# Optimization experiments

Hardware: AMD Instinct MI355X
Metric: run time of the kernel (lower is better)

The kernel has to match this reference:

```python
import jax, jax.numpy as jnp
import numpy as np

B, P, ENC, DEC, EMB, ATT, V, L = 32, 196, 2048, 512, 512, 512, 32000, 21
T = L - 1  # decode steps


def setup_inputs() -> dict:
    key = jax.random.key(0)
    ks = jax.random.split(key, 20)
    u = lambda k, s, a=0.1: jax.random.uniform(k, s, jnp.float32, -a, a)
    lens = jax.random.randint(ks[1], (B, 1), 5, L + 1)
    lens = lens.at[0, 0].set(L)  # force max_decode_len == T (static)
    return {
        'encoder_out': jax.random.normal(ks[0], (B, P, ENC), jnp.float32),
        'encoded_captions': jax.random.randint(ks[2], (B, L), 0, V),
        'caption_lengths': lens,
        'emb_W': u(ks[3], (V, EMB)),
        'W_ea': u(ks[4], (ATT, ENC), 0.02), 'b_ea': jnp.zeros((ATT,)),
        'W_da': u(ks[5], (ATT, DEC), 0.02), 'b_da': jnp.zeros((ATT,)),
        'w_fa': u(ks[6], (1, ATT), 0.02), 'b_fa': jnp.zeros((1,)),
        'W_ih': u(ks[7], (4 * DEC, EMB + ENC), 0.02), 'b_ih': jnp.zeros((4 * DEC,)),
        'W_hh': u(ks[8], (4 * DEC, DEC), 0.02), 'b_hh': jnp.zeros((4 * DEC,)),
        'W_h0': u(ks[9], (DEC, ENC), 0.02), 'b_h0': jnp.zeros((DEC,)),
        'W_c0': u(ks[10], (DEC, ENC), 0.02), 'b_c0': jnp.zeros((DEC,)),
        'W_fb': u(ks[11], (ENC, DEC), 0.02), 'b_fb': jnp.zeros((ENC,)),
        'W_fc': u(ks[12], (V, DEC)), 'b_fc': jnp.zeros((V,)),
    }


def reference(encoder_out, encoded_captions, caption_lengths, emb_W,
              W_ea, b_ea, W_da, b_da, w_fa, b_fa,
              W_ih, b_ih, W_hh, b_hh, W_h0, b_h0, W_c0, b_c0,
              W_fb, b_fb, W_fc, b_fc):
    # sort by caption length descending (as in torch forward)
    lens = caption_lengths[:, 0]
    sort_ind = jnp.argsort(-lens)
    lens_s = lens[sort_ind]
    enc = encoder_out[sort_ind]          # [B,P,ENC]
    caps = encoded_captions[sort_ind]    # [B,L]
    dec_lens = lens_s - 1

    mean_enc = enc.mean(axis=1)
    h0 = mean_enc @ W_h0.T + b_h0
    c0 = mean_enc @ W_c0.T + b_c0

    att1 = jnp.einsum('bpe,ae->bpa', enc, W_ea) + b_ea  # precompute encoder attn proj
    embs = emb_W[caps]                                   # [B,L,EMB]
    emb_seq = jnp.transpose(embs[:, :T], (1, 0, 2))      # [T,B,EMB] (teacher forcing)
    mask_seq = jnp.arange(T)[:, None] < dec_lens[None, :]  # [T,B]

    def step(carry, xs):
        h, c = carry
        emb_t, m = xs  # [B,EMB], [B] bool; m emulates shrinking batch_size_t
        att2 = h @ W_da.T + b_da
        e = jnp.maximum(att1 + att2[:, None, :], 0.0) @ w_fa[0] + b_fa[0]  # [B,P]
        alpha = jax.nn.softmax(e, axis=1)
        awe = jnp.einsum('bp,bpe->be', alpha, enc)
        gate = jax.nn.sigmoid(h @ W_fb.T + b_fb)
        x = jnp.concatenate([emb_t, gate * awe], axis=1)
        g = x @ W_ih.T + b_ih + h @ W_hh.T + b_hh
        i, f, gg, o = jnp.split(g, 4, axis=1)
        c_new = jax.nn.sigmoid(f) * c + jax.nn.sigmoid(i) * jnp.tanh(gg)
        h_new = jax.nn.sigmoid(o) * jnp.tanh(c_new)
        preds = h_new @ W_fc.T + b_fc  # dropout in eval mode (identity)
        mf = m[:, None]
        h = jnp.where(mf, h_new, h)
        c = jnp.where(mf, c_new, c)
        preds = preds * mf.astype(preds.dtype)
        alpha = alpha * mf.astype(alpha.dtype)
        return (h, c), (preds, alpha)

    _, (preds, alphas) = jax.lax.scan(step, (h0, c0), (emb_seq, mask_seq))
    predictions = jnp.transpose(preds, (1, 0, 2))  # [B,T,V]
    alphas = jnp.transpose(alphas, (1, 0, 2))      # [B,T,P]
    return predictions, alphas
```

## Files before the change

### kernel.cpp

```cpp
#include <hip/hip_runtime.h>
#include <hip/hip_bf16.h>
#include <cstddef>

#define NB 32
#define NP 196
#define NE 2048
#define ND 512
#define NV 32000
#define NL 21
#define NT 20

typedef __attribute__((ext_vector_type(8))) short short8;
typedef __attribute__((ext_vector_type(4))) float f32x4;

__device__ __forceinline__ unsigned short f2b(float f) {
    __hip_bfloat16 h = __float2bfloat16(f);
    return *reinterpret_cast<unsigned short*>(&h);
}
__device__ __forceinline__ float b2f_lo(unsigned int u) {
    union { unsigned int i; float f; } v; v.i = u << 16; return v.f;
}
__device__ __forceinline__ float b2f_hi(unsigned int u) {
    union { unsigned int i; float f; } v; v.i = u & 0xffff0000u; return v.f;
}


__global__ void k_sort(const int* __restrict__ lens, int* __restrict__ sind, int* __restrict__ dlens,
                       int* __restrict__ rowmap, int* __restrict__ mpad)
{
    int i = threadIdx.x;
    if (i < NB) {
        int li = lens[i];
        int r = 0;
        for (int j = 0; j < NB; ++j) {
            int lj = lens[j];
            if (lj > li || (lj == li && j < i)) ++r;
        }
        sind[r] = i;
        dlens[r] = li - 1;
    }
    __syncthreads();
    if (i == 0) {
        int c = 0;
        for (int t = 0; t < NT; ++t)
            for (int b = 0; b < NB; ++b)
                if (t < dlens[b]) rowmap[c++] = t * NB + b;
        int pad = (c + 63) & ~63;
        for (int r = c; r < pad; ++r) rowmap[r] = -1;
        mpad[0] = pad;
    }
}

__global__ __launch_bounds__(256) void k_mean(const float* __restrict__ enc, const int* __restrict__ sind,
                                              float* __restrict__ mean_enc)
{
    int b = blockIdx.y;
    int k = blockIdx.x * 256 + threadIdx.x;
    const float* e = enc + (size_t)sind[b] * NP * NE + k;
    float s0 = 0.f, s1 = 0.f, s2 = 0.f, s3 = 0.f;
    for (int p = 0; p < NP; p += 4) {
        s0 += e[(size_t)(p + 0) * NE];
        s1 += e[(size_t)(p + 1) * NE];
        s2 += e[(size_t)(p + 2) * NE];
        s3 += e[(size_t)(p + 3) * NE];
    }
    mean_enc[(size_t)b * NE + k] = (s0 + s1 + s2 + s3) * (1.0f / NP);
}

__global__ __launch_bounds__(256) void k_zero(const int* __restrict__ dlens, float* __restrict__ out)
{
    int b = blockIdx.x / NT, t = blockIdx.x % NT;
    if (t < dlens[b]) return;
    float4 z = {0.f, 0.f, 0.f, 0.f};
    float4* row = (float4*)(out + ((size_t)b * NT + t) * NV);
    for (int i = threadIdx.x; i < NV / 4; i += 256) row[i] = z;
}

__global__ __launch_bounds__(256) void gemm_skinny_split(
    const float* __restrict__ A0, const float* __restrict__ W0a, const float* __restrict__ W0b,
    float* __restrict__ spart)
{
    __shared__ float As[32][32];
    __shared__ float Ws[64][33];
    int n0 = blockIdx.x * 64;
    int ks = blockIdx.y;
    int tid = threadIdx.x;
    int lb = tid / 8, lkq = tid % 8;
    int b4 = (tid / 32) * 4, nl = (tid % 32) * 2;
    float acc[4][2] = {};
    for (int kt = ks * 256; kt < ks * 256 + 256; kt += 32) {
        float4 a4 = *reinterpret_cast<const float4*>(A0 + (size_t)lb * NE + kt + lkq * 4);
        As[lkq * 4 + 0][lb] = a4.x; As[lkq * 4 + 1][lb] = a4.y;
        As[lkq * 4 + 2][lb] = a4.z; As[lkq * 4 + 3][lb] = a4.w;
        #pragma unroll
        for (int r = 0; r < 2; ++r) {
            int s = tid + r * 256;
            int n_l = s / 8, kq = s % 8;
            int ng = n0 + n_l;
            const float* wrow = (ng < 512) ? (W0a + (size_t)ng * NE)
                                           : (W0b + (size_t)(ng - 512) * NE);
            float4 w4 = *reinterpret_cast<const float4*>(wrow + kt + kq * 4);
            Ws[n_l][kq * 4 + 0] = w4.x; Ws[n_l][kq * 4 + 1] = w4.y;
            Ws[n_l][kq * 4 + 2] = w4.z; Ws[n_l][kq * 4 + 3] = w4.w;
        }
        __syncthreads();
        #pragma unroll
        for (int k = 0; k < 32; ++k) {
            float4 av = *reinterpret_cast<const float4*>(&As[k][b4]);
            float w0 = Ws[nl][k], w1 = Ws[nl + 1][k];
            acc[0][0] += av.x * w0; acc[0][1] += av.x * w1;
            acc[1][0] += av.y * w0; acc[1][1] += av.y * w1;
            acc[2][0] += av.z * w0; acc[2][1] += av.z * w1;
            acc[3][0] += av.w * w0; acc[3][1] += av.w * w1;
        }
        __syncthreads();
    }
    float* Cp = spart + (size_t)ks * NB * 1024;
    #pragma unroll
    for (int j = 0; j < 2; ++j)
        #pragma unroll
        for (int i = 0; i < 4; ++i)
            Cp[(size_t)(b4 + i) * 1024 + n0 + nl + j] = acc[i][j];
}

__global__ __launch_bounds__(256) void k_hc0(
    const float* __restrict__ spart, const float* __restrict__ ba, const float* __restrict__ bb,
    float* __restrict__ hc, float* __restrict__ xh)
{
    int b = blockIdx.x;
    for (int ng = threadIdx.x; ng < 1024; ng += 256) {
        float s = (ng < 512) ? ba[ng] : bb[ng - 512];
        #pragma unroll
        for (int ks = 0; ks < 8; ++ks)
            s += spart[(size_t)ks * NB * 1024 + (size_t)b * 1024 + ng];
        hc[(size_t)b * 1024 + ng] = s;
        if (ng < 512) xh[(size_t)b * 3072 + 2560 + ng] = s;
    }
}

__global__ __launch_bounds__(256) void gemm_att1_mfma(
    const float* __restrict__ enc, const float* __restrict__ W_ea,
    const float* __restrict__ bias, unsigned short* __restrict__ att1B,
    const int* __restrict__ sind)
{
    int fid = blockIdx.x;
    int c = fid & 7, x = (fid >> 3) & 7, pg = fid >> 6;
    int p = pg * 8 + c;
    if (p >= 98) return;
    int bm0 = p * 64, bn0 = x * 64;
    __shared__ unsigned short As[64][40];
    __shared__ unsigned short Bs[64][40];
    int tid = threadIdx.x;
    int w = tid >> 6, lane = tid & 63;
    int srow = tid >> 2, schunk = (tid & 3) * 8;
    int mg = bm0 + srow;
    int bidx = mg / NP, pp = mg - bidx * NP;
    const float* arow = enc + ((size_t)sind[bidx] * NP + pp) * NE + schunk;
    const float* brow = W_ea + (size_t)(bn0 + srow) * NE + schunk;
// ... 24 lines not shown
        }
        __syncthreads();
    }
    int crow = bm0 + w * 16 + (lane >> 4) * 4;
    int ccol0 = lane & 15;
    #pragma unroll
    for (int n = 0; n < 4; ++n) {
        int col = bn0 + n * 16 + ccol0;
        float bb2 = bias[col];
        #pragma unroll
        for (int i = 0; i < 4; ++i)
            att1B[(size_t)(crow + i) * ND + col] = f2b(acc[n][i] + bb2);
    }
}

__global__ __launch_bounds__(256) void gemm_preds_mfma(
    const unsigned short* __restrict__ hseqB, const float* __restrict__ W_fc,
    const float* __restrict__ bias, float* __restrict__ out,
    const int* __restrict__ rowmap, const int* __restrict__ mpad)
{
    int fid = blockIdx.x;
    int c = fid & 7;
    int rem = fid >> 3;
    int m = rem % 10, g = rem / 10;
    int n = g * 8 + c;
    if (n >= 250) return;
    int bm0 = m * 64;
    if (bm0 >= mpad[0]) return;
    int bn0 = n * 128;
    __shared__ unsigned short As[64][40];
    __shared__ unsigned short Bs[128][40];
    int tid = threadIdx.x;
    int w = tid >> 6, lane = tid & 63;
    int srow = tid >> 2, schunk = (tid & 3) * 8;
    int rid = rowmap[bm0 + srow];
    const unsigned short* aptr = hseqB + (size_t)(rid < 0 ? 0 : rid) * ND + schunk;
    const float* bptr0 = W_fc + (size_t)(bn0 + srow) * ND + schunk;
    const float* bptr1 = W_fc + (size_t)(bn0 + 64 + srow) * ND + schunk;
    int frow = lane & 15, fk = (lane >> 4) * 8;
    f32x4 acc[8] = {};
    for (int kt = 0; kt < ND; kt += 32) {
        uint4 av = *reinterpret_cast<const uint4*>(aptr + kt);
        float4 c0 = *reinterpret_cast<const float4*>(bptr0 + kt);
        float4 c1 = *reinterpret_cast<const float4*>(bptr0 + kt + 4);
        float4 d0 = *reinterpret_cast<const float4*>(bptr1 + kt);
        float4 d1 = *reinterpret_cast<const float4*>(bptr1 + kt + 4);
        uint4 bv0, bv1;
        bv0.x = f2b(c0.x) | ((unsigned)f2b(c0.y) << 16);
        bv0.y = f2b(c0.z) | ((unsigned)f2b(c0.w) << 16);
        bv0.z = f2b(c1.x) | ((unsigned)f2b(c1.y) << 16);
        bv0.w = f2b(c1.z) | ((unsigned)f2b(c1.w) << 16);
        bv1.x = f2b(d0.x) | ((unsigned)f2b(d0.y) << 16);
        bv1.y = f2b(d0.z) | ((unsigned)f2b(d0.w) << 16);
        bv1.z = f2b(d1.x) | ((unsigned)f2b(d1.y) << 16);
        bv1.w = f2b(d1.z) | ((unsigned)f2b(d1.w) << 16);
        *reinterpret_cast<uint4*>(&As[srow][schunk]) = av;
        *reinterpret_cast<uint4*>(&Bs[srow][schunk]) = bv0;
        *reinterpret_cast<uint4*>(&Bs[64 + srow][schunk]) = bv1;
        __syncthreads();
        short8 af = *reinterpret_cast<const short8*>(&As[w * 16 + frow][fk]);
        #pragma unroll
        for (int nn = 0; nn < 8; ++nn) {
            short8 bf = *reinterpret_cast<const short8*>(&Bs[nn * 16 + frow][fk]);
            acc[nn] = __builtin_amdgcn_mfma_f32_16x16x32_bf16(af, bf, acc[nn], 0, 0, 0);
        }
        __syncthreads();
    }
    int rl0 = w * 16 + (lane >> 4) * 4;
    int ccol0 = lane & 15;
    #pragma unroll
    for (int i = 0; i < 4; ++i) {
        int rm = rowmap[bm0 + rl0 + i];
        if (rm < 0) continue;
        int t = rm / NB, b = rm % NB;
        float* orow = out + ((size_t)b * NT + t) * NV;
        #pragma unroll
        for (int nn = 0; nn < 8; ++nn) {
            int col = bn0 + nn * 16 + ccol0;
            orow[col] = acc[nn][i] + bias[col];
        }
    }
}

__global__ __launch_bounds__(256) void k_attg(
    const float* __restrict__ hc, const float* __restrict__ W_da, const float* __restrict__ W_fb,
    const float* __restrict__ b_da, const float* __restrict__ b_fb, float* __restrict__ attg)
{
    __shared__ float As[32][32];
    __shared__ float Ws[64][33];
    int n0 = blockIdx.x * 64;
    int tid = threadIdx.x;
    int lb = tid / 8, lkq = tid % 8;
    int b4 = (tid / 32) * 4, nl = (tid % 32) * 2;
    float acc[4][2] = {};
    for (int kt = 0; kt < 512; kt += 32) {
        float4 a4 = *reinterpret_cast<const float4*>(hc + (size_t)lb * 1024 + kt + lkq * 4);
        As[lkq * 4 + 0][lb] = a4.x; As[lkq * 4 + 1][lb] = a4.y;
        As[lkq * 4 + 2][lb] = a4.z; As[lkq * 4 + 3][lb] = a4.w;
        #pragma unroll
        for (int r = 0; r < 2; ++r) {
            int s = tid + r * 256;
            int n_l = s / 8, kq = s % 8;
            int ng = n0 + n_l;
            const float* wrow = (ng < 512) ? (W_da + (size_t)ng * 512)
                                           : (W_fb + (size_t)(ng - 512) * 512);
            float4 w4 = *reinterpret_cast<const float4*>(wrow + kt + kq * 4);
            Ws[n_l][kq * 4 + 0] = w4.x; Ws[n_l][kq * 4 + 1] = w4.y;
            Ws[n_l][kq * 4 + 2] = w4.z; Ws[n_l][kq * 4 + 3] = w4.w;
        }
        __syncthreads();
        #pragma unroll
        for (int k = 0; k < 32; ++k) {
            float4 av = *reinterpret_cast<const float4*>(&As[k][b4]);
            float w0 = Ws[nl][k], w1 = Ws[nl + 1][k];
            acc[0][0] += av.x * w0; acc[0][1] += av.x * w1;
            acc[1][0] += av.y * w0; acc[1][1] += av.y * w1;
            acc[2][0] += av.z * w0; acc[2][1] += av.z * w1;
            acc[3][0] += av.w * w0; acc[3][1] += av.w * w1;
        }
        __syncthreads();
    }
    #pragma unroll
    for (int j = 0; j < 2; ++j) {
        int ng = n0 + nl + j;
        float bias = (ng < 512) ? b_da[ng] : b_fb[ng - 512];
        #pragma unroll
        for (int i = 0; i < 4; ++i)
            attg[(size_t)(b4 + i) * 2560 + ng] = acc[i][j] + bias;
    }
}

__global__ __launch_bounds__(256) void k_e(
    const unsigned short* __restrict__ att1B, const float* __restrict__ attg,
    const float* __restrict__ w_fa, const float* __restrict__ b_fa,
    float* __restrict__ e)
{
    __shared__ float att2s[ND];
    __shared__ float wfas[ND];
    int b = blockIdx.y, tid = threadIdx.x;
    const float* ag = attg + (size_t)b * 2560;
    for (int d = tid; d < ND; d += 256) { att2s[d] = ag[d]; wfas[d] = w_fa[d]; }
    __syncthreads();
    int w = tid >> 6, lane = tid & 63;
    int p0 = blockIdx.x * 28;
    const unsigned short* a1 = att1B + ((size_t)b * NP + p0) * ND;
    #pragma unroll
    for (int i = 0; i < 7; ++i) {
        int p = w + 4 * i;
        const unsigned short* row = a1 + (size_t)p * ND;
        float s = 0.f;
        #pragma unroll
        for (int j = 0; j < 2; ++j) {
            int d = j * 256 + lane * 4;
            uint2 u = *reinterpret_cast<const uint2*>(row + d);
            float v0 = b2f_lo(u.x), v1 = b2f_hi(u.x);
            float v2 = b2f_lo(u.y), v3 = b2f_hi(u.y);
            float4 a2 = *reinterpret_cast<const float4*>(&att2s[d]);
            float4 wf = *reinterpret_cast<const float4*>(&wfas[d]);
            s += fmaxf(v0 + a2.x, 0.f) * wf.x + fmaxf(v1 + a2.y, 0.f) * wf.y
               + fmaxf(v2 + a2.z, 0.f) * wf.z + fmaxf(v3 + a2.w, 0.f) * wf.w;
        }
        for (int off = 32; off > 0; off >>= 1) s += __shfl_down(s, off);
        if (lane == 0) e[(size_t)b * NP + p0 + p] = s + b_fa[0];
    }
}

__global__ __launch_bounds__(256) void k_awe(
    const float* __restrict__ enc, const int* __restrict__ sind, const int* __restrict__ dlens,
    const int* __restrict__ caps, const float* __restrict__ emb_W,
    const float* __restrict__ e, const float* __restrict__ attg,
    float* __restrict__ xh, float* __restrict__ out_alpha, int t)
{
    __shared__ float es[256];
    __shared__ float red[256];
    int kc = blockIdx.x, b = blockIdx.y, tid = threadIdx.x;
    float ev = -1e30f;
    if (tid < NP) { float v = e[(size_t)b * NP + tid]; es[tid] = v; ev = v; }
    red[tid] = ev; __syncthreads();
    for (int s2 = 128; s2 > 0; s2 >>= 1) { if (tid < s2) red[tid] = fmaxf(red[tid], red[tid + s2]); __syncthreads(); }
    float m = red[0]; __syncthreads();
    float xe = (tid < NP) ? expf(es[tid] - m) : 0.f;
    red[tid] = xe; __syncthreads();
    for (int s2 = 128; s2 > 0; s2 >>= 1) { if (tid < s2) red[tid] += red[tid + s2]; __syncthreads(); }
    float inv = 1.0f / red[0];
    __syncthreads();
    es[tid] = xe * inv;
    __syncthreads();

    int k = kc * 256 + tid;
    const float* ec = enc + (size_t)sind[b] * NP * NE + k;
    float s0 = 0.f, s1 = 0.f, s2v = 0.f, s3 = 0.f;
    #pragma unroll 4
    for (int p = 0; p < NP; p += 4) {
        s0 += es[p + 0] * ec[(size_t)(p + 0) * NE];
        s1 += es[p + 1] * ec[(size_t)(p + 1) * NE];
        s2v += es[p + 2] * ec[(size_t)(p + 2) * NE];
        s3 += es[p + 3] * ec[(size_t)(p + 3) * NE];
    }
    float awe = (s0 + s1) + (s2v + s3);
    float gp = attg[(size_t)b * 2560 + 512 + k];
    float gate = 1.f / (1.f + expf(-gp));
    xh[(size_t)b * 3072 + 512 + k] = gate * awe;
    if (kc == 0) {
        bool live = (t < dlens[b]);
        if (tid < NP) out_alpha[((size_t)b * NT + t) * NP + tid] = live ? es[tid] : 0.f;
        const float* er = emb_W + (size_t)caps[sind[b] * NL + t] * ND;
        xh[(size_t)b * 3072 + tid] = er[tid];
        xh[(size_t)b * 3072 + 256 + tid] = er[256 + tid];
    }
}

__global__ __launch_bounds__(256) void k_gates(
    const float* __restrict__ xh, const float* __restrict__ W_ih, const float* __restrict__ W_hh,
    float* __restrict__ gpart)
{
    __shared__ float smem[3200];
    int blk = blockIdx.x, tid = threadIdx.x;
    int nt = blk & 31, ks = blk >> 5;
    float* As = smem;
    float (*Ws)[33] = (float(*)[33])(smem + 1024);
    int n0 = nt * 64;
    int lb = tid / 8, lkq = tid % 8;
    int b4 = (tid / 32) * 4, nl = (tid % 32) * 2;
    float acc[4][2] = {};
    for (int kt = ks * 768; kt < ks * 768 + 768; kt += 32) {
        float4 a4 = *reinterpret_cast<const float4*>(xh + (size_t)lb * 3072 + kt + lkq * 4);
        As[(lkq * 4 + 0) * 32 + lb] = a4.x; As[(lkq * 4 + 1) * 32 + lb] = a4.y;
        As[(lkq * 4 + 2) * 32 + lb] = a4.z; As[(lkq * 4 + 3) * 32 + lb] = a4.w;
        #pragma unroll
        for (int r = 0; r < 2; ++r) {
            int s = tid + r * 256;
            int n_l = s / 8, kq = s % 8;
            int ng = n0 + n_l;
            int kk = kt + kq * 4;
            const float* wrow = (kk < 2560) ? (W_ih + (size_t)ng * 2560 + kk)
                                            : (W_hh + (size_t)ng * 512 + (kk - 2560));
            float4 w4 = *reinterpret_cast<const float4*>(wrow);
            Ws[n_l][kq * 4 + 0] = w4.x; Ws[n_l][kq * 4 + 1] = w4.y;
            Ws[n_l][kq * 4 + 2] = w4.z; Ws[n_l][kq * 4 + 3] = w4.w;
        }
        __syncthreads();
        #pragma unroll
        for (int k = 0; k < 32; ++k) {
            float4 av = *reinterpret_cast<const float4*>(&As[k * 32 + b4]);
            float w0 = Ws[nl][k], w1 = Ws[nl + 1][k];
            acc[0][0] += av.x * w0; acc[0][1] += av.x * w1;
            acc[1][0] += av.y * w0; acc[1][1] += av.y * w1;
            acc[2][0] += av.z * w0; acc[2][1] += av.z * w1;
            acc[3][0] += av.w * w0; acc[3][1] += av.w * w1;
        }
        __syncthreads();
    }
    float* Cp = gpart + (size_t)ks * NB * 2048;
    #pragma unroll
    for (int j = 0; j < 2; ++j)
        #pragma unroll
        for (int i = 0; i < 4; ++i)
            Cp[(size_t)(b4 + i) * 2048 + n0 + nl + j] = acc[i][j];
}

__global__ __launch_bounds__(256) void k_cell(
    const float* __restrict__ gpart, const int* __restrict__ dlens,
    const float* __restrict__ b_ih, const float* __restrict__ b_hh,
    float* __restrict__ hc, unsigned short* __restrict__ hseqB, float* __restrict__ xh, int t)
{
    int b = blockIdx.x;
    for (int d = threadIdx.x; d < ND; d += 256) {
        float g0 = b_ih[d] + b_hh[d];
        float g1 = b_ih[512 + d] + b_hh[512 + d];
        float g2 = b_ih[1024 + d] + b_hh[1024 + d];
        float g3 = b_ih[1536 + d] + b_hh[1536 + d];
        #pragma unroll
        for (int ks = 0; ks < 4; ++ks) {
            const float* gp = gpart + ((size_t)ks * NB + b) * 2048;
            g0 += gp[d]; g1 += gp[512 + d]; g2 += gp[1024 + d]; g3 += gp[1536 + d];
        }
        float ig = 1.f / (1.f + expf(-g0));
        float fg = 1.f / (1.f + expf(-g1));
        float gt = tanhf(g2);
        float og = 1.f / (1.f + expf(-g3));
        float c_old = hc[(size_t)b * 1024 + 512 + d];
        float c_new = fg * c_old + ig * gt;
        float h_new = og * tanhf(c_new);
        hseqB[((size_t)t * NB + b) * ND + d] = f2b(h_new);
        if (t < dlens[b]) {
            hc[(size_t)b * 1024 + d] = h_new;
            hc[(size_t)b * 1024 + 512 + d] = c_new;
            xh[(size_t)b * 3072 + 2560 + d] = h_new;
        }
    }
}

extern "C" void kernel_launch(void* const* d_in, const int* in_sizes, int n_in,
                              void* d_out, int out_size, void* d_ws, size_t ws_size,
                              hipStream_t stream)
{
    const float* enc   = (const float*)d_in[0];
    const int*   caps  = (const int*)d_in[1];
    const int*   clens = (const int*)d_in[2];
    const float* emb_W = (const float*)d_in[3];
    const float* W_ea  = (const float*)d_in[4];
    const float* b_ea  = (const float*)d_in[5];
    const float* W_da  = (const float*)d_in[6];
    const float* b_da  = (const float*)d_in[7];
    const float* w_fa  = (const float*)d_in[8];
    const float* b_fa  = (const float*)d_in[9];
    const float* W_ih  = (const float*)d_in[10];
    const float* b_ih  = (const float*)d_in[11];
    const float* W_hh  = (const float*)d_in[12];
    const float* b_hh  = (const float*)d_in[13];
    const float* W_h0  = (const float*)d_in[14];
    const float* b_h0  = (const float*)d_in[15];
    const float* W_c0  = (const float*)d_in[16];
    const float* b_c0  = (const float*)d_in[17];
    const float* W_fb  = (const float*)d_in[18];
    const float* b_fb  = (const float*)d_in[19];
    const float* W_fc  = (const float*)d_in[20];
    const float* b_fc  = (const float*)d_in[21];

    float* out = (float*)d_out;
    float* out_alpha = out + (size_t)NB * NT * NV;

    int* iws    = (int*)d_ws;
    int* sind   = iws;
    int* dlens  = iws + 32;
    int* rowmap = iws + 64;
    int* mpad   = iws + 704;
    float* base = (float*)d_ws + 1024;
    float* mean_enc = base;
    float* hc    = mean_enc + NB * NE;
    float* attg  = hc + NB * 1024;
    float* xh    = attg + NB * 2560;
    float* e     = xh + NB * 3072;
    float* gpart = e + NB * NP;
    unsigned short* att1B = (unsigned short*)(gpart + 4 * NB * 2048);
    unsigned short* hseqB = att1B + (size_t)NB * NP * ND;

    k_sort<<<1, 64, 0, stream>>>(clens, sind, dlens, rowmap, mpad);
    k_zero<<<NB * NT, 256, 0, stream>>>(dlens, out);
    k_mean<<<dim3(NE / 256, NB), 256, 0, stream>>>(enc, sind, mean_enc);
    gemm_skinny_split<<<dim3(16, 8), 256, 0, stream>>>(mean_enc, W_h0, W_c0, gpart);
    k_hc0<<<dim3(NB), 256, 0, stream>>>(gpart, b_h0, b_c0, hc, xh);
    gemm_att1_mfma<<<dim3(832), 256, 0, stream>>>(enc, W_ea, b_ea, att1B, sind);

    for (int t = 0; t < NT; ++t) {
        k_attg<<<dim3(40), 256, 0, stream>>>(hc, W_da, W_fb, b_da, b_fb, attg);
        k_e<<<dim3(7, NB), 256, 0, stream>>>(att1B, attg, w_fa, b_fa, e);
        k_awe<<<dim3(8, NB), 256, 0, stream>>>(enc, sind, dlens, caps, emb_W,
                                               e, attg, xh, out_alpha, t);
        k_gates<<<dim3(128), 256, 0, stream>>>(xh, W_ih, W_hh, gpart);
        k_cell<<<dim3(NB), 256, 0, stream>>>(gpart, dlens, b_ih, b_hh, hc, hseqB, xh, t);
    }

    gemm_preds_mfma<<<dim3(2560), 256, 0, stream>>>(hseqB, W_fc, b_fc, out, rowmap, mpad);
}
```

Baseline: 1.778 ms.

## Fuse LSTM cell into attention-gate GEMM and score into softmax/awe kernel

Cuts the per-step launch count from five kernels to three. The LSTM cell update moves into the start of the attention-gate GEMM: each block recomputes the cell for all batches into shared bf16, block 0 writes the h/c state to a double-buffered array, and a final k_fin kernel handles the last step. Attention scores are now computed inside the softmax/awe kernel, and each of its 8 column blocks redundantly recomputes all 196 scores. k_gates drops its split-K partial buffer and accumulates with atomicAdd into a gates buffer that the attention kernel pre-initializes with biases; this makes float summation order nondeterministic and uses bf16 h as the GEMM input.

```diff
diff --git a/kernel.cpp b/kernel.cpp
--- a/kernel.cpp
+++ b/kernel.cpp
@@ -264,21 +264,55 @@
     }
 }
 
-__global__ __launch_bounds__(256) void k_attg(
-    const float* __restrict__ hc, const float* __restrict__ W_da, const float* __restrict__ W_fb,
-    const float* __restrict__ b_da, const float* __restrict__ b_fb, float* __restrict__ attg)
-{
-    __shared__ float As[32][32];
+__global__ __launch_bounds__(256) void k_attgcell(
+    const float* __restrict__ gates, const int* __restrict__ dlens,
+    const float* __restrict__ W_da, const float* __restrict__ W_fb,
+    const float* __restrict__ b_da, const float* __restrict__ b_fb,
+    float* __restrict__ hcbuf, float* __restrict__ attg,
+    unsigned short* __restrict__ hseqB, float* __restrict__ xh, int t)
+{
+    __shared__ unsigned short hBT[512][36];
     __shared__ float Ws[64][33];
+    int tid = threadIdx.x;
+    const float* hcR = hcbuf + (size_t)((t > 0 ? (t - 1) : 0) & 1) * NB * 1024;
+    if (t == 0) {
+        for (int i = 0; i < 64; ++i) {
+            int idx = i * 256 + tid, b = idx >> 9, d = idx & 511;
+            hBT[d][b] = f2b(hcR[(size_t)b * 1024 + d]);
+        }
+    } else {
+        float* hcW = hcbuf + (size_t)(t & 1) * NB * 1024;
+        bool blk0 = (blockIdx.x == 0);
+        for (int i = 0; i < 64; ++i) {
+            int idx = i * 256 + tid, b = idx >> 9, d = idx & 511;
+            const float* gb = gates + (size_t)b * 2048;
+            float g0 = gb[d], g1 = gb[512 + d], g2 = gb[1024 + d], g3 = gb[1536 + d];
+            float ig = 1.f / (1.f + expf(-g0));
+            float fg = 1.f / (1.f + expf(-g1));
+            float gt = tanhf(g2);
+            float og = 1.f / (1.f + expf(-g3));
+            float h_old = hcR[(size_t)b * 1024 + d];
+            float c_old = hcR[(size_t)b * 1024 + 512 + d];
+            float c_new = fg * c_old + ig * gt;
+            float h_new = og * tanhf(c_new);
+            bool live = (t - 1) < dlens[b];
+            float hv = live ? h_new : h_old;
+            float cv = live ? c_new : c_old;
+            hBT[d][b] = f2b(hv);
+            if (blk0) {
+                hcW[(size_t)b * 1024 + d] = hv;
+                hcW[(size_t)b * 1024 + 512 + d] = cv;
+                hseqB[((size_t)(t - 1) * NB + b) * ND + d] = f2b(h_new);
+                xh[(size_t)b * 3072 + 2560 + d] = hv;
+            }
+        }
+    }
+    __syncthreads();
+
     int n0 = blockIdx.x * 64;
-    int tid = threadIdx.x;
-    int lb = tid / 8, lkq = tid % 8;
     int b4 = (tid / 32) * 4, nl = (tid % 32) * 2;
     float acc[4][2] = {};
     for (int kt = 0; kt < 512; kt += 32) {
-        float4 a4 = *reinterpret_cast<const float4*>(hc + (size_t)lb * 1024 + kt + lkq * 4);
-        As[lkq * 4 + 0][lb] = a4.x; As[lkq * 4 + 1][lb] = a4.y;
-        As[lkq * 4 + 2][lb] = a4.z; As[lkq * 4 + 3][lb] = a4.w;
         #pragma unroll
         for (int r = 0; r < 2; ++r) {
             int s = tid + r * 256;
@@ -293,12 +327,14 @@
         __syncthreads();
         #pragma unroll
         for (int k = 0; k < 32; ++k) {
-            float4 av = *reinterpret_cast<const float4*>(&As[k][b4]);
+            uint2 u = *reinterpret_cast<const uint2*>(&hBT[kt + k][b4]);
+            float a0 = b2f_lo(u.x), a1 = b2f_hi(u.x);
+            float a2 = b2f_lo(u.y), a3 = b2f_hi(u.y);
             float w0 = Ws[nl][k], w1 = Ws[nl + 1][k];
-            acc[0][0] += av.x * w0; acc[0][1] += av.x * w1;
-            acc[1][0] += av.y * w0; acc[1][1] += av.y * w1;
-            acc[2][0] += av.z * w0; acc[2][1] += av.z * w1;
-            acc[3][0] += av.w * w0; acc[3][1] += av.w * w1;
+            acc[0][0] += a0 * w0; acc[0][1] += a0 * w1;
+            acc[1][0] += a1 * w0; acc[1][1] += a1 * w1;
+            acc[2][0] += a2 * w0; acc[2][1] += a2 * w1;
+            acc[3][0] += a3 * w0; acc[3][1] += a3 * w1;
         }
         __syncthreads();
     }
@@ -312,62 +348,55 @@
     }
 }
 
-__global__ __launch_bounds__(256) void k_e(
+__global__ __launch_bounds__(256) void k_att(
+    const float* __restrict__ enc, const int* __restrict__ sind, const int* __restrict__ dlens,
+    const int* __restrict__ caps, const float* __restrict__ emb_W,
     const unsigned short* __restrict__ att1B, const float* __restrict__ attg,
     const float* __restrict__ w_fa, const float* __restrict__ b_fa,
-    float* __restrict__ e)
-{
-    __shared__ float att2s[ND];
-    __shared__ float wfas[ND];
-    int b = blockIdx.y, tid = threadIdx.x;
-    const float* ag = attg + (size_t)b * 2560;
-    for (int d = tid; d < ND; d += 256) { att2s[d] = ag[d]; wfas[d] = w_fa[d]; }
-    __syncthreads();
-    int w = tid >> 6, lane = tid & 63;
-    int p0 = blockIdx.x * 28;
-    const unsigned short* a1 = att1B + ((size_t)b * NP + p0) * ND;
-    #pragma unroll
-    for (int i = 0; i < 7; ++i) {
-        int p = w + 4 * i;
-        const unsigned short* row = a1 + (size_t)p * ND;
-        float s = 0.f;
-        #pragma unroll
-        for (int j = 0; j < 2; ++j) {
-            int d = j * 256 + lane * 4;
-            uint2 u = *reinterpret_cast<const uint2*>(row + d);
-            float v0 = b2f_lo(u.x), v1 = b2f_hi(u.x);
-            float v2 = b2f_lo(u.y), v3 = b2f_hi(u.y);
-            float4 a2 = *reinterpret_cast<const float4*>(&att2s[d]);
-            float4 wf = *reinterpret_cast<const float4*>(&wfas[d]);
-            s += fmaxf(v0 + a2.x, 0.f) * wf.x + fmaxf(v1 + a2.y, 0.f) * wf.y
-               + fmaxf(v2 + a2.z, 0.f) * wf.z + fmaxf(v3 + a2.w, 0.f) * wf.w;
-        }
-        for (int off = 32; off > 0; off >>= 1) s += __shfl_down(s, off);
-        if (lane == 0) e[(size_t)b * NP + p0 + p] = s + b_fa[0];
-    }
-}
-
-__global__ __launch_bounds__(256) void k_awe(
-    const float* __restrict__ enc, const int* __restrict__ sind, const int* __restrict__ dlens,
-    const int* __restrict__ caps, const float* __restrict__ emb_W,
-    const float* __restrict__ e, const float* __restrict__ attg,
-    float* __restrict__ xh, float* __restrict__ out_alpha, int t)
-{
+    const float* __restrict__ b_ih, const float* __restrict__ b_hh,
+    float* __restrict__ xh, float* __restrict__ gates,
+    float* __restrict__ out_alpha, int t)
+{
+    __shared__ float att2s[512];
+    __shared__ float wfas[512];
     __shared__ float es[256];
     __shared__ float red[256];
     int kc = blockIdx.x, b = blockIdx.y, tid = threadIdx.x;
+    const float* ag = attg + (size_t)b * 2560;
+    att2s[tid] = ag[tid]; att2s[256 + tid] = ag[256 + tid];
+    wfas[tid] = w_fa[tid]; wfas[256 + tid] = w_fa[256 + tid];
+    __syncthreads();
     float ev = -1e30f;
-    if (tid < NP) { float v = e[(size_t)b * NP + tid]; es[tid] = v; ev = v; }
+    if (tid < NP) {
+        const unsigned short* row = att1B + ((size_t)b * NP + tid) * ND;
+        float s0 = 0.f, s1 = 0.f;
+        #pragma unroll 8
+        for (int d = 0; d < 512; d += 8) {
+            uint4 u = *reinterpret_cast<const uint4*>(row + d);
+            s0 += fmaxf(b2f_lo(u.x) + att2s[d + 0], 0.f) * wfas[d + 0];
+            s1 += fmaxf(b2f_hi(u.x) + att2s[d + 1], 0.f) * wfas[d + 1];
+            s0 += fmaxf(b2f_lo(u.y) + att2s[d + 2], 0.f) * wfas[d + 2];
+            s1 += fmaxf(b2f_hi(u.y) + att2s[d + 3], 0.f) * wfas[d + 3];
+            s0 += fmaxf(b2f_lo(u.z) + att2s[d + 4], 0.f) * wfas[d + 4];
+            s1 += fmaxf(b2f_hi(u.z) + att2s[d + 5], 0.f) * wfas[d + 5];
+            s0 += fmaxf(b2f_lo(u.w) + att2s[d + 6], 0.f) * wfas[d + 6];
+            s1 += fmaxf(b2f_hi(u.w) + att2s[d + 7], 0.f) * wfas[d + 7];
+        }
+        ev = s0 + s1 + b_fa[0];
+    }
     red[tid] = ev; __syncthreads();
     for (int s2 = 128; s2 > 0; s2 >>= 1) { if (tid < s2) red[tid] = fmaxf(red[tid], red[tid + s2]); __syncthreads(); }
     float m = red[0]; __syncthreads();
-    float xe = (tid < NP) ? expf(es[tid] - m) : 0.f;
+    float xe = (tid < NP) ? expf(ev - m) : 0.f;
     red[tid] = xe; __syncthreads();
     for (int s2 = 128; s2 > 0; s2 >>= 1) { if (tid < s2) red[tid] += red[tid + s2]; __syncthreads(); }
     float inv = 1.0f / red[0];
     __syncthreads();
     es[tid] = xe * inv;
     __syncthreads();
+
+    int n = kc * 256 + tid;
+    gates[(size_t)b * 2048 + n] = b_ih[n] + b_hh[n];
 
     int k = kc * 256 + tid;
     const float* ec = enc + (size_t)sind[b] * NP * NE + k;
@@ -380,7 +409,7 @@
         s3 += es[p + 3] * ec[(size_t)(p + 3) * NE];
     }
     float awe = (s0 + s1) + (s2v + s3);
-    float gp = attg[(size_t)b * 2560 + 512 + k];
+    float gp = ag[512 + k];
     float gate = 1.f / (1.f + expf(-gp));
     xh[(size_t)b * 3072 + 512 + k] = gate * awe;
     if (kc == 0) {
@@ -394,7 +423,7 @@
 
 __global__ __launch_bounds__(256) void k_gates(
     const float* __restrict__ xh, const float* __restrict__ W_ih, const float* __restrict__ W_hh,
-    float* __restrict__ gpart)
+    float* __restrict__ gates)
 {
     __shared__ float smem[3200];
     int blk = blockIdx.x, tid = threadIdx.x;
@@ -433,43 +462,30 @@
         }
         __syncthreads();
     }
-    float* Cp = gpart + (size_t)ks * NB * 2048;
     #pragma unroll
     for (int j = 0; j < 2; ++j)
         #pragma unroll
         for (int i = 0; i < 4; ++i)
-            Cp[(size_t)(b4 + i) * 2048 + n0 + nl + j] = acc[i][j];
-}
-
-__global__ __launch_bounds__(256) void k_cell(
-    const float* __restrict__ gpart, const int* __restrict__ dlens,
-    const float* __restrict__ b_ih, const float* __restrict__ b_hh,
-    float* __restrict__ hc, unsigned short* __restrict__ hseqB, float* __restrict__ xh, int t)
+            atomicAdd(&gates[(size_t)(b4 + i) * 2048 + n0 + nl + j], acc[i][j]);
+}
+
+__global__ __launch_bounds__(256) void k_fin(
+    const float* __restrict__ gates, const float* __restrict__ hcbuf,
+    unsigned short* __restrict__ hseqB)
 {
     int b = blockIdx.x;
+    const float* hcR = hcbuf + (size_t)((NT - 1) & 1) * NB * 1024 + (size_t)b * 1024;
+    const float* gb = gates + (size_t)b * 2048;
     for (int d = threadIdx.x; d < ND; d += 256) {
-        float g0 = b_ih[d] + b_hh[d];
-        float g1 = b_ih[512 + d] + b_hh[512 + d];
-        float g2 = b_ih[1024 + d] + b_hh[1024 + d];
-        float g3 = b_ih[1536 + d] + b_hh[1536 + d];
-        #pragma unroll
-        for (int ks = 0; ks < 4; ++ks) {
-            const float* gp = gpart + ((size_t)ks * NB + b) * 2048;
-            g0 += gp[d]; g1 += gp[512 + d]; g2 += gp[1024 + d]; g3 += gp[1536 + d];
-        }
+        float g0 = gb[d], g1 = gb[512 + d], g2 = gb[1024 + d], g3 = gb[1536 + d];
         float ig = 1.f / (1.f + expf(-g0));
         float fg = 1.f / (1.f + expf(-g1));
         float gt = tanhf(g2);
         float og = 1.f / (1.f + expf(-g3));
-        float c_old = hc[(size_t)b * 1024 + 512 + d];
+        float c_old = hcR[512 + d];
         float c_new = fg * c_old + ig * gt;
         float h_new = og * tanhf(c_new);
-        hseqB[((size_t)t * NB + b) * ND + d] = f2b(h_new);
-        if (t < dlens[b]) {
-            hc[(size_t)b * 1024 + d] = h_new;
-            hc[(size_t)b * 1024 + 512 + d] = c_new;
-            xh[(size_t)b * 3072 + 2560 + d] = h_new;
-        }
+        hseqB[((size_t)(NT - 1) * NB + b) * ND + d] = f2b(h_new);
     }
 }
 
@@ -510,29 +526,29 @@
     int* mpad   = iws + 704;
     float* base = (float*)d_ws + 1024;
     float* mean_enc = base;
-    float* hc    = mean_enc + NB * NE;
-    float* attg  = hc + NB * 1024;
+    float* hcbuf = mean_enc + NB * NE;
+    float* attg  = hcbuf + 2 * NB * 1024;
     float* xh    = attg + NB * 2560;
-    float* e     = xh + NB * 3072;
-    float* gpart = e + NB * NP;
-    unsigned short* att1B = (unsigned short*)(gpart + 4 * NB * 2048);
+    float* gates = xh + NB * 3072;
+    unsigned short* att1B = (unsigned short*)(gates + 262144);
     unsigned short* hseqB = att1B + (size_t)NB * NP * ND;
 
     k_sort<<<1, 64, 0, stream>>>(clens, sind, dlens, rowmap, mpad);
     k_zero<<<NB * NT, 256, 0, stream>>>(dlens, out);
     k_mean<<<dim3(NE / 256, NB), 256, 0, stream>>>(enc, sind, mean_enc);
-    gemm_skinny_split<<<dim3(16, 8), 256, 0, stream>>>(mean_enc, W_h0, W_c0, gpart);
-    k_hc0<<<dim3(NB), 256, 0, stream>>>(gpart, b_h0, b_c0, hc, xh);
+    gemm_skinny_split<<<dim3(16, 8), 256, 0, stream>>>(mean_enc, W_h0, W_c0, gates);
+    k_hc0<<<dim3(NB), 256, 0, stream>>>(gates, b_h0, b_c0, hcbuf, xh);
     gemm_att1_mfma<<<dim3(832), 256, 0, stream>>>(enc, W_ea, b_ea, att1B, sind);
 
     for (int t = 0; t < NT; ++t) {
-        k_attg<<<dim3(40), 256, 0, stream>>>(hc, W_da, W_fb, b_da, b_fb, attg);
-        k_e<<<dim3(7, NB), 256, 0, stream>>>(att1B, attg, w_fa, b_fa, e);
-        k_awe<<<dim3(8, NB), 256, 0, stream>>>(enc, sind, dlens, caps, emb_W,
-                                               e, attg, xh, out_alpha, t);
-        k_gates<<<dim3(128), 256, 0, stream>>>(xh, W_ih, W_hh, gpart);
-        k_cell<<<dim3(NB), 256, 0, stream>>>(gpart, dlens, b_ih, b_hh, hc, hseqB, xh, t);
-    }
+        k_attgcell<<<dim3(40), 256, 0, stream>>>(gates, dlens, W_da, W_fb, b_da, b_fb,
+                                                 hcbuf, attg, hseqB, xh, t);
+        k_att<<<dim3(8, NB), 256, 0, stream>>>(enc, sind, dlens, caps, emb_W,
+                                               att1B, attg, w_fa, b_fa, b_ih, b_hh,
+                                               xh, gates, out_alpha, t);
+        k_gates<<<dim3(128), 256, 0, stream>>>(xh, W_ih, W_hh, gates);
+    }
+    k_fin<<<dim3(NB), 256, 0, stream>>>(gates, hcbuf, hseqB);
 
     gemm_preds_mfma<<<dim3(2560), 256, 0, stream>>>(hseqB, W_fc, b_fc, out, rowmap, mpad);
 }
```

Measured after the change: 2.760 ms. +55.2%, slower.

## Store recurrent weights in bf16 and fuse attention score into awe kernel

Applied to the files above, without the earlier changes.

Converts W_da/W_fb and W_ih/W_hh to bf16 once per call, so the per-step attg and gates GEMMs read half the weight bytes from memory. It also merges k_e into k_awe, so each awe block recomputes all 196 attention scores for its batch row in shared memory rather than writing them to global and launching a separate kernel. The cost is an extra conversion pass over about 7 MB of weights each call, reduced weight precision, and an 8x duplication of score computation across the kc blocks.

```diff
diff --git a/kernel.cpp b/kernel.cpp
--- a/kernel.cpp
+++ b/kernel.cpp
@@ -74,6 +74,44 @@
     float4 z = {0.f, 0.f, 0.f, 0.f};
     float4* row = (float4*)(out + ((size_t)b * NT + t) * NV);
     for (int i = threadIdx.x; i < NV / 4; i += 256) row[i] = z;
+}
+
+__global__ __launch_bounds__(256) void k_conv_df(
+    const float* __restrict__ W_da, const float* __restrict__ W_fb,
+    unsigned short* __restrict__ wdfB)
+{
+    int idx = (blockIdx.x * 256 + threadIdx.x) * 8;
+    if (idx >= 2560 * 512) return;
+    int n = idx >> 9, k = idx & 511;
+    const float* src = (n < 512) ? (W_da + (size_t)n * 512 + k)
+                                 : (W_fb + (size_t)(n - 512) * 512 + k);
+    float4 a = *reinterpret_cast<const float4*>(src);
+    float4 b = *reinterpret_cast<const float4*>(src + 4);
+    uint4 o;
+    o.x = f2b(a.x) | ((unsigned)f2b(a.y) << 16);
+    o.y = f2b(a.z) | ((unsigned)f2b(a.w) << 16);
+    o.z = f2b(b.x) | ((unsigned)f2b(b.y) << 16);
+    o.w = f2b(b.z) | ((unsigned)f2b(b.w) << 16);
+    *reinterpret_cast<uint4*>(wdfB + idx) = o;
+}
+
+__global__ __launch_bounds__(256) void k_conv_xh(
+    const float* __restrict__ W_ih, const float* __restrict__ W_hh,
+    unsigned short* __restrict__ wxhB)
+{
+    int idx = (blockIdx.x * 256 + threadIdx.x) * 8;
+    if (idx >= 2048 * 3072) return;
+    int n = idx / 3072, kk = idx % 3072;
+    const float* src = (kk < 2560) ? (W_ih + (size_t)n * 2560 + kk)
+                                   : (W_hh + (size_t)n * 512 + (kk - 2560));
+    float4 a = *reinterpret_cast<const float4*>(src);
+    float4 b = *reinterpret_cast<const float4*>(src + 4);
+    uint4 o;
+    o.x = f2b(a.x) | ((unsigned)f2b(a.y) << 16);
+    o.y = f2b(a.z) | ((unsigned)f2b(a.w) << 16);
+    o.z = f2b(b.x) | ((unsigned)f2b(b.y) << 16);
+    o.w = f2b(b.z) | ((unsigned)f2b(b.w) << 16);
+    *reinterpret_cast<uint4*>(wxhB + idx) = o;
 }
 
 __global__ __launch_bounds__(256) void gemm_skinny_split(
@@ -265,7 +303,7 @@
 }
 
 __global__ __launch_bounds__(256) void k_attg(
-    const float* __restrict__ hc, const float* __restrict__ W_da, const float* __restrict__ W_fb,
+    const float* __restrict__ hc, const unsigned short* __restrict__ wdfB,
     const float* __restrict__ b_da, const float* __restrict__ b_fb, float* __restrict__ attg)
 {
     __shared__ float As[32][32];
@@ -273,23 +311,18 @@
     int n0 = blockIdx.x * 64;
     int tid = threadIdx.x;
     int lb = tid / 8, lkq = tid % 8;
+    int wn = tid >> 2, wk = (tid & 3) * 8;
     int b4 = (tid / 32) * 4, nl = (tid % 32) * 2;
     float acc[4][2] = {};
     for (int kt = 0; kt < 512; kt += 32) {
         float4 a4 = *reinterpret_cast<const float4*>(hc + (size_t)lb * 1024 + kt + lkq * 4);
         As[lkq * 4 + 0][lb] = a4.x; As[lkq * 4 + 1][lb] = a4.y;
         As[lkq * 4 + 2][lb] = a4.z; As[lkq * 4 + 3][lb] = a4.w;
-        #pragma unroll
-        for (int r = 0; r < 2; ++r) {
-            int s = tid + r * 256;
-            int n_l = s / 8, kq = s % 8;
-            int ng = n0 + n_l;
-            const float* wrow = (ng < 512) ? (W_da + (size_t)ng * 512)
-                                           : (W_fb + (size_t)(ng - 512) * 512);
-            float4 w4 = *reinterpret_cast<const float4*>(wrow + kt + kq * 4);
-            Ws[n_l][kq * 4 + 0] = w4.x; Ws[n_l][kq * 4 + 1] = w4.y;
-            Ws[n_l][kq * 4 + 2] = w4.z; Ws[n_l][kq * 4 + 3] = w4.w;
-        }
+        uint4 u = *reinterpret_cast<const uint4*>(wdfB + (size_t)(n0 + wn) * 512 + kt + wk);
+        Ws[wn][wk + 0] = b2f_lo(u.x); Ws[wn][wk + 1] = b2f_hi(u.x);
+        Ws[wn][wk + 2] = b2f_lo(u.y); Ws[wn][wk + 3] = b2f_hi(u.y);
+        Ws[wn][wk + 4] = b2f_lo(u.z); Ws[wn][wk + 5] = b2f_hi(u.z);
+        Ws[wn][wk + 6] = b2f_lo(u.w); Ws[wn][wk + 7] = b2f_hi(u.w);
         __syncthreads();
         #pragma unroll
         for (int k = 0; k < 32; ++k) {
@@ -312,63 +345,52 @@
     }
 }
 
-__global__ __launch_bounds__(256) void k_e(
+__global__ __launch_bounds__(256) void k_eawe(
+    const float* __restrict__ enc, const int* __restrict__ sind, const int* __restrict__ dlens,
+    const int* __restrict__ caps, const float* __restrict__ emb_W,
     const unsigned short* __restrict__ att1B, const float* __restrict__ attg,
     const float* __restrict__ w_fa, const float* __restrict__ b_fa,
-    float* __restrict__ e)
-{
-    __shared__ float att2s[ND];
-    __shared__ float wfas[ND];
-    int b = blockIdx.y, tid = threadIdx.x;
-    const float* ag = attg + (size_t)b * 2560;
-    for (int d = tid; d < ND; d += 256) { att2s[d] = ag[d]; wfas[d] = w_fa[d]; }
-    __syncthreads();
-    int w = tid >> 6, lane = tid & 63;
-    int p0 = blockIdx.x * 28;
-    const unsigned short* a1 = att1B + ((size_t)b * NP + p0) * ND;
-    #pragma unroll
-    for (int i = 0; i < 7; ++i) {
-        int p = w + 4 * i;
-        const unsigned short* row = a1 + (size_t)p * ND;
-        float s = 0.f;
-        #pragma unroll
-        for (int j = 0; j < 2; ++j) {
-            int d = j * 256 + lane * 4;
-            uint2 u = *reinterpret_cast<const uint2*>(row + d);
-            float v0 = b2f_lo(u.x), v1 = b2f_hi(u.x);
-            float v2 = b2f_lo(u.y), v3 = b2f_hi(u.y);
-            float4 a2 = *reinterpret_cast<const float4*>(&att2s[d]);
-            float4 wf = *reinterpret_cast<const float4*>(&wfas[d]);
-            s += fmaxf(v0 + a2.x, 0.f) * wf.x + fmaxf(v1 + a2.y, 0.f) * wf.y
-               + fmaxf(v2 + a2.z, 0.f) * wf.z + fmaxf(v3 + a2.w, 0.f) * wf.w;
-        }
-        for (int off = 32; off > 0; off >>= 1) s += __shfl_down(s, off);
-        if (lane == 0) e[(size_t)b * NP + p0 + p] = s + b_fa[0];
-    }
-}
-
-__global__ __launch_bounds__(256) void k_awe(
-    const float* __restrict__ enc, const int* __restrict__ sind, const int* __restrict__ dlens,
-    const int* __restrict__ caps, const float* __restrict__ emb_W,
-    const float* __restrict__ e, const float* __restrict__ attg,
     float* __restrict__ xh, float* __restrict__ out_alpha, int t)
 {
+    __shared__ float att2s[512];
+    __shared__ float wfas[512];
     __shared__ float es[256];
     __shared__ float red[256];
     int kc = blockIdx.x, b = blockIdx.y, tid = threadIdx.x;
-    float ev = -1e30f;
-    if (tid < NP) { float v = e[(size_t)b * NP + tid]; es[tid] = v; ev = v; }
+    const float* ag = attg + (size_t)b * 2560;
+    att2s[tid] = ag[tid]; att2s[256 + tid] = ag[256 + tid];
+    wfas[tid] = w_fa[tid]; wfas[256 + tid] = w_fa[256 + tid];
+    __syncthreads();
+    int w = tid >> 6, lane = tid & 63;
+    float bfa = b_fa[0];
+    int d0 = lane * 8;
+    const unsigned short* a1 = att1B + (size_t)b * NP * ND;
+    for (int i = 0; i < 49; ++i) {
+        int p = w + 4 * i;
+        uint4 u = *reinterpret_cast<const uint4*>(a1 + (size_t)p * ND + d0);
+        float s = fmaxf(b2f_lo(u.x) + att2s[d0 + 0], 0.f) * wfas[d0 + 0]
+                + fmaxf(b2f_hi(u.x) + att2s[d0 + 1], 0.f) * wfas[d0 + 1]
+                + fmaxf(b2f_lo(u.y) + att2s[d0 + 2], 0.f) * wfas[d0 + 2]
+                + fmaxf(b2f_hi(u.y) + att2s[d0 + 3], 0.f) * wfas[d0 + 3]
+                + fmaxf(b2f_lo(u.z) + att2s[d0 + 4], 0.f) * wfas[d0 + 4]
+                + fmaxf(b2f_hi(u.z) + att2s[d0 + 5], 0.f) * wfas[d0 + 5]
+                + fmaxf(b2f_lo(u.w) + att2s[d0 + 6], 0.f) * wfas[d0 + 6]
+                + fmaxf(b2f_hi(u.w) + att2s[d0 + 7], 0.f) * wfas[d0 + 7];
+        for (int off = 32; off > 0; off >>= 1) s += __shfl_down(s, off);
+        if (lane == 0) es[p] = s + bfa;
+    }
+    __syncthreads();
+    float ev = (tid < NP) ? es[tid] : -1e30f;
     red[tid] = ev; __syncthreads();
     for (int s2 = 128; s2 > 0; s2 >>= 1) { if (tid < s2) red[tid] = fmaxf(red[tid], red[tid + s2]); __syncthreads(); }
     float m = red[0]; __syncthreads();
-    float xe = (tid < NP) ? expf(es[tid] - m) : 0.f;
+    float xe = (tid < NP) ? expf(ev - m) : 0.f;
     red[tid] = xe; __syncthreads();
     for (int s2 = 128; s2 > 0; s2 >>= 1) { if (tid < s2) red[tid] += red[tid + s2]; __syncthreads(); }
     float inv = 1.0f / red[0];
     __syncthreads();
     es[tid] = xe * inv;
     __syncthreads();
-
     int k = kc * 256 + tid;
     const float* ec = enc + (size_t)sind[b] * NP * NE + k;
     float s0 = 0.f, s1 = 0.f, s2v = 0.f, s3 = 0.f;
@@ -380,7 +402,7 @@
         s3 += es[p + 3] * ec[(size_t)(p + 3) * NE];
     }
     float awe = (s0 + s1) + (s2v + s3);
-    float gp = attg[(size_t)b * 2560 + 512 + k];
+    float gp = ag[512 + k];
     float gate = 1.f / (1.f + expf(-gp));
     xh[(size_t)b * 3072 + 512 + k] = gate * awe;
     if (kc == 0) {
@@ -393,7 +415,7 @@
 }
 
 __global__ __launch_bounds__(256) void k_gates(
-    const float* __restrict__ xh, const float* __restrict__ W_ih, const float* __restrict__ W_hh,
+    const float* __restrict__ xh, const unsigned short* __restrict__ wxhB,
     float* __restrict__ gpart)
 {
     __shared__ float smem[3200];
@@ -403,24 +425,18 @@
     float (*Ws)[33] = (float(*)[33])(smem + 1024);
     int n0 = nt * 64;
     int lb = tid / 8, lkq = tid % 8;
+    int wn = tid >> 2, wk = (tid & 3) * 8;
     int b4 = (tid / 32) * 4, nl = (tid % 32) * 2;
     float acc[4][2] = {};
     for (int kt = ks * 768; kt < ks * 768 + 768; kt += 32) {
         float4 a4 = *reinterpret_cast<const float4*>(xh + (size_t)lb * 3072 + kt + lkq * 4);
         As[(lkq * 4 + 0) * 32 + lb] = a4.x; As[(lkq * 4 + 1) * 32 + lb] = a4.y;
         As[(lkq * 4 + 2) * 32 + lb] = a4.z; As[(lkq * 4 + 3) * 32 + lb] = a4.w;
-        #pragma unroll
-        for (int r = 0; r < 2; ++r) {
-            int s = tid + r * 256;
-            int n_l = s / 8, kq = s % 8;
-            int ng = n0 + n_l;
-            int kk = kt + kq * 4;
-            const float* wrow = (kk < 2560) ? (W_ih + (size_t)ng * 2560 + kk)
-                                            : (W_hh + (size_t)ng * 512 + (kk - 2560));
-            float4 w4 = *reinterpret_cast<const float4*>(wrow);
-            Ws[n_l][kq * 4 + 0] = w4.x; Ws[n_l][kq * 4 + 1] = w4.y;
-            Ws[n_l][kq * 4 + 2] = w4.z; Ws[n_l][kq * 4 + 3] = w4.w;
-        }
+        uint4 u = *reinterpret_cast<const uint4*>(wxhB + (size_t)(n0 + wn) * 3072 + kt + wk);
+        Ws[wn][wk + 0] = b2f_lo(u.x); Ws[wn][wk + 1] = b2f_hi(u.x);
+        Ws[wn][wk + 2] = b2f_lo(u.y); Ws[wn][wk + 3] = b2f_hi(u.y);
+        Ws[wn][wk + 4] = b2f_lo(u.z); Ws[wn][wk + 5] = b2f_hi(u.z);
+        Ws[wn][wk + 6] = b2f_lo(u.w); Ws[wn][wk + 7] = b2f_hi(u.w);
         __syncthreads();
         #pragma unroll
         for (int k = 0; k < 32; ++k) {
@@ -513,24 +529,27 @@
     float* hc    = mean_enc + NB * NE;
     float* attg  = hc + NB * 1024;
     float* xh    = attg + NB * 2560;
-    float* e     = xh + NB * 3072;
-    float* gpart = e + NB * NP;
-    unsigned short* att1B = (unsigned short*)(gpart + 4 * NB * 2048);
+    float* gpart = xh + NB * 3072;
+    unsigned short* att1B = (unsigned short*)(gpart + 262144);
     unsigned short* hseqB = att1B + (size_t)NB * NP * ND;
+    unsigned short* wdfB  = hseqB + (size_t)NT * NB * ND;
+    unsigned short* wxhB  = wdfB + (size_t)2560 * 512;
 
     k_sort<<<1, 64, 0, stream>>>(clens, sind, dlens, rowmap, mpad);
     k_zero<<<NB * NT, 256, 0, stream>>>(dlens, out);
+    k_conv_df<<<dim3(640), 256, 0, stream>>>(W_da, W_fb, wdfB);
+    k_conv_xh<<<dim3(3072), 256, 0, stream>>>(W_ih, W_hh, wxhB);
     k_mean<<<dim3(NE / 256, NB), 256, 0, stream>>>(enc, sind, mean_enc);
     gemm_skinny_split<<<dim3(16, 8), 256, 0, stream>>>(mean_enc, W_h0, W_c0, gpart);
     k_hc0<<<dim3(NB), 256, 0, stream>>>(gpart, b_h0, b_c0, hc, xh);
     gemm_att1_mfma<<<dim3(832), 256, 0, stream>>>(enc, W_ea, b_ea, att1B, sind);
 
     for (int t = 0; t < NT; ++t) {
-        k_attg<<<dim3(40), 256, 0, stream>>>(hc, W_da, W_fb, b_da, b_fb, attg);
-        k_e<<<dim3(7, NB), 256, 0, stream>>>(att1B, attg, w_fa, b_fa, e);
-        k_awe<<<dim3(8, NB), 256, 0, stream>>>(enc, sind, dlens, caps, emb_W,
-                                               e, attg, xh, out_alpha, t);
-        k_gates<<<dim3(128), 256, 0, stream>>>(xh, W_ih, W_hh, gpart);
+        k_attg<<<dim3(40), 256, 0, stream>>>(hc, wdfB, b_da, b_fb, attg);
+        k_eawe<<<dim3(8, NB), 256, 0, stream>>>(enc, sind, dlens, caps, emb_W,
+                                                att1B, attg, w_fa, b_fa,
+                                                xh, out_alpha, t);
+        k_gates<<<dim3(128), 256, 0, stream>>>(xh, wxhB, gpart);
         k_cell<<<dim3(NB), 256, 0, stream>>>(gpart, dlens, b_ih, b_hh, hc, hseqB, xh, t);
     }
 
```

New measurement: 2.139 ms. 1.2x slower.

## Fuse LSTM cell into gates GEMM via atomic split-K and grid counter

Applied to the files above, without the earlier changes.

The separate k_cell launch is removed. Split-K partial results from k_gates are now accumulated with float atomicAdd into a gates buffer, which k_awe pre-fills with the biases. A global arrival counter with an agent-scope spin wait lets the first 32 blocks run the LSTM cell update once all 128 blocks have contributed. This saves one kernel launch and one round-trip through the partial-sum buffer per decode step. In exchange it relies on all 128 blocks being co-resident, uses atomic float adds whose summation order is not deterministic, and has a bounded spin that could break out early.

```diff
diff --git a/kernel.cpp b/kernel.cpp
--- a/kernel.cpp
+++ b/kernel.cpp
@@ -26,7 +26,7 @@
 
 
 __global__ void k_sort(const int* __restrict__ lens, int* __restrict__ sind, int* __restrict__ dlens,
-                       int* __restrict__ rowmap, int* __restrict__ mpad)
+                       int* __restrict__ rowmap, int* __restrict__ mpad, unsigned* __restrict__ cnt)
 {
     int i = threadIdx.x;
     if (i < NB) {
@@ -48,6 +48,7 @@
         int pad = (c + 63) & ~63;
         for (int r = c; r < pad; ++r) rowmap[r] = -1;
         mpad[0] = pad;
+        cnt[0] = 0u;
     }
 }
 
@@ -351,7 +352,9 @@
     const float* __restrict__ enc, const int* __restrict__ sind, const int* __restrict__ dlens,
     const int* __restrict__ caps, const float* __restrict__ emb_W,
     const float* __restrict__ e, const float* __restrict__ attg,
-    float* __restrict__ xh, float* __restrict__ out_alpha, int t)
+    const float* __restrict__ b_ih, const float* __restrict__ b_hh,
+    float* __restrict__ xh, float* __restrict__ gates,
+    float* __restrict__ out_alpha, int t)
 {
     __shared__ float es[256];
     __shared__ float red[256];
@@ -369,6 +372,9 @@
     es[tid] = xe * inv;
     __syncthreads();
 
+    int n = kc * 256 + tid;
+    gates[(size_t)b * 2048 + n] = b_ih[n] + b_hh[n];
+
     int k = kc * 256 + tid;
     const float* ec = enc + (size_t)sind[b] * NP * NE + k;
     float s0 = 0.f, s1 = 0.f, s2v = 0.f, s3 = 0.f;
@@ -394,7 +400,8 @@
 
 __global__ __launch_bounds__(256) void k_gates(
     const float* __restrict__ xh, const float* __restrict__ W_ih, const float* __restrict__ W_hh,
-    float* __restrict__ gpart)
+    float* __restrict__ gates, unsigned* __restrict__ cnt, const int* __restrict__ dlens,
+    float* __restrict__ hc, unsigned short* __restrict__ hseqB, float* __restrict__ xhw, int t)
 {
     __shared__ float smem[3200];
     int blk = blockIdx.x, tid = threadIdx.x;
@@ -433,30 +440,32 @@
         }
         __syncthreads();
     }
-    float* Cp = gpart + (size_t)ks * NB * 2048;
     #pragma unroll
     for (int j = 0; j < 2; ++j)
         #pragma unroll
         for (int i = 0; i < 4; ++i)
-            Cp[(size_t)(b4 + i) * 2048 + n0 + nl + j] = acc[i][j];
-}
-
-__global__ __launch_bounds__(256) void k_cell(
-    const float* __restrict__ gpart, const int* __restrict__ dlens,
-    const float* __restrict__ b_ih, const float* __restrict__ b_hh,
-    float* __restrict__ hc, unsigned short* __restrict__ hseqB, float* __restrict__ xh, int t)
-{
-    int b = blockIdx.x;
-    for (int d = threadIdx.x; d < ND; d += 256) {
-        float g0 = b_ih[d] + b_hh[d];
-        float g1 = b_ih[512 + d] + b_hh[512 + d];
-        float g2 = b_ih[1024 + d] + b_hh[1024 + d];
-        float g3 = b_ih[1536 + d] + b_hh[1536 + d];
-        #pragma unroll
-        for (int ks = 0; ks < 4; ++ks) {
-            const float* gp = gpart + ((size_t)ks * NB + b) * 2048;
-            g0 += gp[d]; g1 += gp[512 + d]; g2 += gp[1024 + d]; g3 += gp[1536 + d];
-        }
+            atomicAdd(&gates[(size_t)(b4 + i) * 2048 + n0 + nl + j], acc[i][j]);
+
+    __syncthreads();
+    if (tid == 0)
+        __hip_atomic_fetch_add(cnt, 1u, __ATOMIC_ACQ_REL, __HIP_MEMORY_SCOPE_AGENT);
+    if (blk >= 32) return;
+    if (tid == 0) {
+        unsigned target = 128u * (unsigned)(t + 1);
+        unsigned iters = 0;
+        while (__hip_atomic_load(cnt, __ATOMIC_ACQUIRE, __HIP_MEMORY_SCOPE_AGENT) < target) {
+            __builtin_amdgcn_s_sleep(1);
+            if (++iters > 200000000u) break;
+        }
+    }
+    __syncthreads();
+    int b = blk;
+    bool live = (t < dlens[b]);
+    for (int d = tid; d < ND; d += 256) {
+        float g0 = __hip_atomic_load(&gates[(size_t)b * 2048 + d],        __ATOMIC_RELAXED, __HIP_MEMORY_SCOPE_AGENT);
+        float g1 = __hip_atomic_load(&gates[(size_t)b * 2048 + 512 + d],  __ATOMIC_RELAXED, __HIP_MEMORY_SCOPE_AGENT);
+        float g2 = __hip_atomic_load(&gates[(size_t)b * 2048 + 1024 + d], __ATOMIC_RELAXED, __HIP_MEMORY_SCOPE_AGENT);
+        float g3 = __hip_atomic_load(&gates[(size_t)b * 2048 + 1536 + d], __ATOMIC_RELAXED, __HIP_MEMORY_SCOPE_AGENT);
         float ig = 1.f / (1.f + expf(-g0));
         float fg = 1.f / (1.f + expf(-g1));
         float gt = tanhf(g2);
@@ -465,10 +474,10 @@
         float c_new = fg * c_old + ig * gt;
         float h_new = og * tanhf(c_new);
         hseqB[((size_t)t * NB + b) * ND + d] = f2b(h_new);
-        if (t < dlens[b]) {
+        if (live) {
             hc[(size_t)b * 1024 + d] = h_new;
             hc[(size_t)b * 1024 + 512 + d] = c_new;
-            xh[(size_t)b * 3072 + 2560 + d] = h_new;
+            xhw[(size_t)b * 3072 + 2560 + d] = h_new;
         }
     }
 }
@@ -508,30 +517,32 @@
     int* dlens  = iws + 32;
     int* rowmap = iws + 64;
     int* mpad   = iws + 704;
+    unsigned* cnt = (unsigned*)(iws + 706);
     float* base = (float*)d_ws + 1024;
     float* mean_enc = base;
     float* hc    = mean_enc + NB * NE;
     float* attg  = hc + NB * 1024;
     float* xh    = attg + NB * 2560;
     float* e     = xh + NB * 3072;
-    float* gpart = e + NB * NP;
-    unsigned short* att1B = (unsigned short*)(gpart + 4 * NB * 2048);
+    float* gates = e + NB * NP + 128;
+    unsigned short* att1B = (unsigned short*)(gates + 262144);
     unsigned short* hseqB = att1B + (size_t)NB * NP * ND;
 
-    k_sort<<<1, 64, 0, stream>>>(clens, sind, dlens, rowmap, mpad);
+    k_sort<<<1, 64, 0, stream>>>(clens, sind, dlens, rowmap, mpad, cnt);
     k_zero<<<NB * NT, 256, 0, stream>>>(dlens, out);
     k_mean<<<dim3(NE / 256, NB), 256, 0, stream>>>(enc, sind, mean_enc);
-    gemm_skinny_split<<<dim3(16, 8), 256, 0, stream>>>(mean_enc, W_h0, W_c0, gpart);
-    k_hc0<<<dim3(NB), 256, 0, stream>>>(gpart, b_h0, b_c0, hc, xh);
+    gemm_skinny_split<<<dim3(16, 8), 256, 0, stream>>>(mean_enc, W_h0, W_c0, gates);
+    k_hc0<<<dim3(NB), 256, 0, stream>>>(gates, b_h0, b_c0, hc, xh);
     gemm_att1_mfma<<<dim3(832), 256, 0, stream>>>(enc, W_ea, b_ea, att1B, sind);
 
     for (int t = 0; t < NT; ++t) {
         k_attg<<<dim3(40), 256, 0, stream>>>(hc, W_da, W_fb, b_da, b_fb, attg);
         k_e<<<dim3(7, NB), 256, 0, stream>>>(att1B, attg, w_fa, b_fa, e);
         k_awe<<<dim3(8, NB), 256, 0, stream>>>(enc, sind, dlens, caps, emb_W,
-                                               e, attg, xh, out_alpha, t);
-        k_gates<<<dim3(128), 256, 0, stream>>>(xh, W_ih, W_hh, gpart);
-        k_cell<<<dim3(NB), 256, 0, stream>>>(gpart, dlens, b_ih, b_hh, hc, hseqB, xh, t);
+                                               e, attg, b_ih, b_hh,
+                                               xh, gates, out_alpha, t);
+        k_gates<<<dim3(128), 256, 0, stream>>>(xh, W_ih, W_hh, gates, cnt, dlens,
+                                               hc, hseqB, xh, t);
     }
 
     gemm_preds_mfma<<<dim3(2560), 256, 0, stream>>>(hseqB, W_fc, b_fc, out, rowmap, mpad);
```

Result: no change. 1.813 ms (+2.0%).
